# Kernel optimization log

Measured on AMD Instinct MI355X. Metric: run time of the kernel, lower is better.

The kernel has to match this reference:

```python
import jax, jax.numpy as jnp
import numpy as np
import math

D_MODEL = 1024
N_HEADS = 16
D_K = D_MODEL // N_HEADS
THRESH = 0.1  # attention probs below this are zeroed


def setup_inputs() -> dict:
    key = jax.random.key(0)
    ks = jax.random.split(key, 9)
    B, S, D = 2, 2048, D_MODEL
    scale = 1.0 / math.sqrt(D)
    x = jax.random.normal(ks[0], (B, S, D), dtype=jnp.float32)
    Wq = jax.random.normal(ks[1], (D, D), dtype=jnp.float32) * scale
    bq = jax.random.normal(ks[2], (D,), dtype=jnp.float32) * 0.01
    Wk = jax.random.normal(ks[3], (D, D), dtype=jnp.float32) * scale
    bk = jax.random.normal(ks[4], (D,), dtype=jnp.float32) * 0.01
    Wv = jax.random.normal(ks[5], (D, D), dtype=jnp.float32) * scale
    bv = jax.random.normal(ks[6], (D,), dtype=jnp.float32) * 0.01
    Wo = jax.random.normal(ks[7], (D, D), dtype=jnp.float32) * scale
    bo = jax.random.normal(ks[8], (D,), dtype=jnp.float32) * 0.01
    return {"x": x, "Wq": Wq, "bq": bq, "Wk": Wk, "bk": bk,
            "Wv": Wv, "bv": bv, "Wo": Wo, "bo": bo}


def _split_heads(t):
    B, S, D = t.shape
    return t.reshape(B, S, N_HEADS, D_K).transpose(0, 2, 1, 3)  # [B,H,S,dk]


def reference(x, Wq, bq, Wk, bk, Wv, bv, Wo, bo):
    # torch nn.Linear: y = x @ W.T + b
    q = _split_heads(x @ Wq.T + bq)
    k = _split_heads(x @ Wk.T + bk)
    v = _split_heads(x @ Wv.T + bv)
    scores = jnp.einsum('bhqd,bhkd->bhqk', q, k) / math.sqrt(D_K)
    probs = jax.nn.softmax(scores, axis=-1)          # full unmasked softmax (returned)
    keep = probs >= THRESH                            # ~low_attention_mask
    probs_model = jnp.where(keep, probs, 0.0)        # masked_fill; dropout is identity in eval
    ctx = jnp.einsum('bhqk,bhkd->bhqd', probs_model, v)
    B, H, S, dk = ctx.shape
    merged = ctx.transpose(0, 2, 1, 3).reshape(B, S, H * dk)
    out = merged @ Wo.T + bo
    attention_sum = probs.sum(axis=1)                # [B,S,S] sum over heads
    attention_mask = keep.astype(jnp.float32).sum(axis=1)  # [B,S,S]
    return (out, attention_sum, attention_mask)
```

## Files before the change

### kernel.cpp

```cpp
#include <hip/hip_runtime.h>

#define SDIM 2048
#define DDIM 1024
#define NH 16
#define DK 64
#define NB 2
#define MROWS (NB * SDIM)
#define MAXEV 65536
#define EXPC 0.18033688011112f

typedef _Float16 f16x8 __attribute__((ext_vector_type(8)));
typedef _Float16 f16x4 __attribute__((ext_vector_type(4)));
typedef float f32x4 __attribute__((ext_vector_type(4)));

__device__ __forceinline__ void ld_lds16(const _Float16* g, _Float16* l) {
  __builtin_amdgcn_global_load_lds(
      (const __attribute__((address_space(1))) void*)g,
      (__attribute__((address_space(3))) void*)l, 16, 0, 0);
}

__global__ __launch_bounds__(256) void cvt_f16(
    const float* __restrict__ x, const float* __restrict__ wq,
    const float* __restrict__ wk, const float* __restrict__ wv,
    _Float16* __restrict__ xh, _Float16* __restrict__ wqh,
    _Float16* __restrict__ wkh, _Float16* __restrict__ wvh) {
  int i = blockIdx.x * 256 + threadIdx.x;
  const float* src;
  _Float16* dst;
  int off;
  if (i < 1048576) {
    src = x; dst = xh; off = i;
  } else if (i < 1310720) {
    src = wq; dst = wqh; off = i - 1048576;
  } else if (i < 1572864) {
    src = wk; dst = wkh; off = i - 1310720;
  } else {
    src = wv; dst = wvh; off = i - 1572864;
  }
  float4 v = ((const float4*)src)[off];
  f16x4 h;
  h[0] = (_Float16)v.x; h[1] = (_Float16)v.y;
  h[2] = (_Float16)v.z; h[3] = (_Float16)v.w;
  ((f16x4*)dst)[off] = h;
}

__global__ __launch_bounds__(256, 2) void proj_gemm(
    const _Float16* __restrict__ xh, const _Float16* __restrict__ Wqh,
    const _Float16* __restrict__ Wkh, const _Float16* __restrict__ Wvh,
    const float* __restrict__ bq, const float* __restrict__ bk,
    const float* __restrict__ bv, _Float16* __restrict__ Qo,
    _Float16* __restrict__ Ko, float* __restrict__ Vo) {
  __shared__ _Float16 sA[128 * 64];
  __shared__ _Float16 sB[128 * 64];
  const int t = threadIdx.x;
  const int lane = t & 63, wv = t >> 6;
  const int lr = lane & 15, quad = lane >> 4;
  const int wm = wv >> 1, wn = wv & 1;
  const int m0 = blockIdx.y * 128, n0 = blockIdx.x * 128;
  const int z = blockIdx.z;
  const _Float16* Bp = z == 0 ? Wqh : (z == 1 ? Wkh : Wvh);
  const float* bias = z == 0 ? bq : (z == 1 ? bk : bv);

  const int strow = t >> 3;
  const int stchunk = t & 7;
  const int stsrc = (stchunk ^ (strow & 7)) * 8;

  f32x4 acc[4][4];
#pragma unroll
  for (int i = 0; i < 4; ++i)
#pragma unroll
    for (int j = 0; j < 4; ++j) acc[i][j] = (f32x4){0.f, 0.f, 0.f, 0.f};

  for (int k0 = 0; k0 < DDIM; k0 += 64) {
    __syncthreads();
#pragma unroll
    for (int i = 0; i < 4; ++i) {
      const int row = i * 32 + strow;
      ld_lds16(&xh[(size_t)(m0 + row) * DDIM + k0 + stsrc],
               &sA[row * 64 + stchunk * 8]);
      ld_lds16(&Bp[(size_t)(n0 + row) * DDIM + k0 + stsrc],
               &sB[row * 64 + stchunk * 8]);
    }
    __syncthreads();
    f16x8 af[4][2], bf[4][2];
#pragma unroll
    for (int i = 0; i < 4; ++i)
#pragma unroll
      for (int kk = 0; kk < 2; ++kk) {
        const int ph = ((kk * 4 + quad) ^ (lr & 7)) * 8;
        af[i][kk] = *(const f16x8*)&sA[(wm * 64 + i * 16 + lr) * 64 + ph];
        bf[i][kk] = *(const f16x8*)&sB[(wn * 64 + i * 16 + lr) * 64 + ph];
      }
#pragma unroll
    for (int kk = 0; kk < 2; ++kk)
#pragma unroll
      for (int i = 0; i < 4; ++i)
#pragma unroll
        for (int j = 0; j < 4; ++j)
          acc[i][j] = __builtin_amdgcn_mfma_f32_16x16x32_f16(
              af[i][kk], bf[j][kk], acc[i][j], 0, 0, 0);
  }
#pragma unroll
  for (int j = 0; j < 4; ++j) {
    const int ng = n0 + wn * 64 + j * 16 + lr;
    const float bvv = bias[ng];
    const int h = ng >> 6, d = ng & 63;
#pragma unroll
    for (int i = 0; i < 4; ++i) {
#pragma unroll
      for (int r = 0; r < 4; ++r) {
        const int mg = m0 + wm * 64 + i * 16 + quad * 4 + r;
        const int b = mg >> 11, s = mg & 2047;
        const float o = acc[i][j][r] + bvv;
        const size_t off = ((size_t)(b * NH + h) * SDIM + s) * DK + d;
        if (z == 0)
          Qo[off] = (_Float16)o;
        else if (z == 1)
          Ko[off] = (_Float16)o;
        else
          Vo[off] = o;
      }
    }
  }
}

__global__ __launch_bounds__(256) void attn_denom(const _Float16* __restrict__ Q,
                                                  const _Float16* __restrict__ K,
                                                  float* __restrict__ invDen) {
  __shared__ _Float16 Kbuf[2 * 64 * 64];
  const int t = threadIdx.x;
  const int lane = t & 63, wave = t >> 6;
  const int quad = lane >> 4, lr = lane & 15;
  const int q0 = blockIdx.x * 64;
  const int bh = blockIdx.y;
  const _Float16* Qh = Q + (size_t)bh * SDIM * DK;
  const _Float16* Kh = K + (size_t)bh * SDIM * DK;
  const size_t qoff = (size_t)(q0 + wave * 16 + lr) * DK + quad * 8;
  const f16x8 aq0 = *(const f16x8*)&Qh[qoff];
  const f16x8 aq1 = *(const f16x8*)&Qh[qoff + 32];
  const int strow = t >> 3, stchunk = t & 7;
  const int stsrc = (stchunk ^ (strow & 7)) * 8;
  const int ph0 = (quad ^ (lr & 7)) * 8;
  const int ph1 = ((4 + quad) ^ (lr & 7)) * 8;

  float dsum[4] = {0.f, 0.f, 0.f, 0.f};
#pragma unroll
  for (int i = 0; i < 2; ++i)
    ld_lds16(&Kh[(size_t)(i * 32 + strow) * DK + stsrc],
             &Kbuf[(i * 32 + strow) * 64 + stchunk * 8]);

  for (int kt = 0; kt < 32; ++kt) {
    __syncthreads();
    if (kt + 1 < 32) {
      const int kn = (kt + 1) * 64;
      const int bsel = ((kt + 1) & 1) * 4096;
#pragma unroll
      for (int i = 0; i < 2; ++i)
        ld_lds16(&Kh[(size_t)(kn + i * 32 + strow) * DK + stsrc],
                 &Kbuf[bsel + (i * 32 + strow) * 64 + stchunk * 8]);
    }
    const _Float16* Ks = &Kbuf[(kt & 1) * 4096];
#pragma unroll
    for (int c = 0; c < 4; ++c) {
      f16x8 b0 = *(const f16x8*)&Ks[(c * 16 + lr) * 64 + ph0];
      f16x8 b1 = *(const f16x8*)&Ks[(c * 16 + lr) * 64 + ph1];
      f32x4 acc = {0.f, 0.f, 0.f, 0.f};
      acc = __builtin_amdgcn_mfma_f32_16x16x32_f16(aq0, b0, acc, 0, 0, 0);
      acc = __builtin_amdgcn_mfma_f32_16x16x32_f16(aq1, b1, acc, 0, 0, 0);
#pragma unroll
      for (int r = 0; r < 4; ++r)
        dsum[r] += exp2f(acc[r] * EXPC);
    }
  }
#pragma unroll
  for (int m = 1; m < 16; m <<= 1)
#pragma unroll
    for (int r = 0; r < 4; ++r)
      dsum[r] += __shfl_xor(dsum[r], m, 64);
  if (lr == 0) {
#pragma unroll
    for (int r = 0; r < 4; ++r)
      invDen[(size_t)bh * SDIM + q0 + wave * 16 + quad * 4 + r] =
          1.0f / dsum[r];
  }
}

__global__ __launch_bounds__(256) void attn_pass2(
    const _Float16* __restrict__ Q, const _Float16* __restrict__ K,
    const float* __restrict__ invDen, float* __restrict__ attSum,
    float* __restrict__ attMask, float4* __restrict__ ev,
    int* __restrict__ ecnt) {
  __shared__ float Tbuf[64 * 68];
  _Float16* Kbuf = (_Float16*)Tbuf;
  const int t = threadIdx.x;
  const int lane = t & 63, wave = t >> 6;
  const int quad = lane >> 4, lr = lane & 15;
  const int k0 = blockIdx.x * 64;
  const int q0 = blockIdx.y * 64;
  const int b = blockIdx.z;
  const int strow = t >> 3, stchunk = t & 7;
  const int stsrc = (stchunk ^ (strow & 7)) * 8;
  const int ph0 = (quad ^ (lr & 7)) * 8;
  const int ph1 = ((4 + quad) ^ (lr & 7)) * 8;

  const size_t qbase = ((size_t)(b * NH) * SDIM + q0 + wave * 16 + lr) * DK;
  const size_t dbase = (size_t)(b * NH) * SDIM + q0 + wave * 16 + quad * 4;
  const size_t hstep = (size_t)SDIM * DK;

  float asum[4][4] = {};
  float amask[4][4] = {};

  {
    const _Float16* Kh = K + (size_t)(b * NH) * hstep + (size_t)k0 * DK;
#pragma unroll
    for (int i = 0; i < 2; ++i)
      ld_lds16(&Kh[(size_t)(i * 32 + strow) * DK + stsrc],
               &Kbuf[(i * 32 + strow) * 64 + stchunk * 8]);
  }
  f16x8 aq0n = *(const f16x8*)&Q[qbase + quad * 8];
  f16x8 aq1n = *(const f16x8*)&Q[qbase + 32 + quad * 8];
  float4 iln = *(const float4*)&invDen[dbase];

#pragma unroll 1
  for (int h = 0; h < NH; ++h) {
    const f16x8 aq0 = aq0n, aq1 = aq1n;
    const float4 il4 = iln;
    __syncthreads();
    if (h + 1 < NH) {
      const _Float16* Kn =
          K + (size_t)(b * NH + h + 1) * hstep + (size_t)k0 * DK;
      const int bsel = ((h + 1) & 1) * 4096;
#pragma unroll
      for (int i = 0; i < 2; ++i)
        ld_lds16(&Kn[(size_t)(i * 32 + strow) * DK + stsrc],
                 &Kbuf[bsel + (i * 32 + strow) * 64 + stchunk * 8]);
      aq0n = *(const f16x8*)&Q[qbase + (size_t)(h + 1) * hstep + quad * 8];
      aq1n = *(const f16x8*)&Q[qbase + (size_t)(h + 1) * hstep + 32 + quad * 8];
      iln = *(const float4*)&invDen[dbase + (size_t)(h + 1) * SDIM];
    }
    const _Float16* Ks = &Kbuf[(h & 1) * 4096];
    const float il[4] = {il4.x, il4.y, il4.z, il4.w};
#pragma unroll
    for (int c = 0; c < 4; ++c) {
      f16x8 b0 = *(const f16x8*)&Ks[(c * 16 + lr) * 64 + ph0];
      f16x8 b1 = *(const f16x8*)&Ks[(c * 16 + lr) * 64 + ph1];
      f32x4 acc = {0.f, 0.f, 0.f, 0.f};
      acc = __builtin_amdgcn_mfma_f32_16x16x32_f16(aq0, b0, acc, 0, 0, 0);
      acc = __builtin_amdgcn_mfma_f32_16x16x32_f16(aq1, b1, acc, 0, 0, 0);
#pragma unroll
      for (int r = 0; r < 4; ++r) {
        float p = exp2f(acc[r] * EXPC) * il[r];
        asum[c][r] += p;
        if (p >= 0.1f) {
          amask[c][r] += 1.0f;
          int idx = atomicAdd(ecnt, 1);
          if (idx < MAXEV)
            ev[idx] = make_float4(
                __int_as_float(b * NH + h),
                __int_as_float(q0 + wave * 16 + quad * 4 + r),
                __int_as_float(k0 + c * 16 + lr), p);
        }
      }
    }
  }
  const int orow = t >> 2, ocol = (t & 3) * 16;
  __syncthreads();
#pragma unroll
  for (int c = 0; c < 4; ++c)
#pragma unroll
    for (int r = 0; r < 4; ++r)
      Tbuf[(wave * 16 + quad * 4 + r) * 68 + c * 16 + lr] = asum[c][r];
  __syncthreads();
#pragma unroll
  for (int j = 0; j < 4; ++j) {
    float4 v = *(float4*)&Tbuf[orow * 68 + ocol + j * 4];
    *(float4*)&attSum[((size_t)(b * SDIM) + q0 + orow) * SDIM + k0 + ocol +
                      j * 4] = v;
  }
  __syncthreads();
#pragma unroll
  for (int c = 0; c < 4; ++c)
#pragma unroll
    for (int r = 0; r < 4; ++r)
      Tbuf[(wave * 16 + quad * 4 + r) * 68 + c * 16 + lr] = amask[c][r];
  __syncthreads();
#pragma unroll
  for (int j = 0; j < 4; ++j) {
    float4 v = *(float4*)&Tbuf[orow * 68 + ocol + j * 4];
    *(float4*)&attMask[((size_t)(b * SDIM) + q0 + orow) * SDIM + k0 + ocol +
                       j * 4] = v;
  }
}

__global__ __launch_bounds__(64) void apply_events(
    const float4* __restrict__ ev, const int* __restrict__ ecnt,
    const float* __restrict__ V, float* __restrict__ merged,
    int* __restrict__ flags) {
  int n = *ecnt;
  if (n > MAXEV) n = MAXEV;
  const int d = threadIdx.x;
  for (int e = blockIdx.x; e < n; e += gridDim.x) {
    float4 r = ev[e];
    int bh = __float_as_int(r.x);
    int q = __float_as_int(r.y);
    int kc = __float_as_int(r.z);
    float p = r.w;
    int b = bh >> 4, h = bh & 15;
    atomicAdd(&merged[((size_t)(b * SDIM + q)) * DDIM + h * DK + d],
              p * V[((size_t)bh * SDIM + kc) * DK + d]);
    if (d == 0) flags[b * SDIM + q] = 1;
  }
}

__global__ __launch_bounds__(256) void out_gemm(const float* __restrict__ A,
                                                const float* __restrict__ W,
                                                const float* __restrict__ bias,
                                                float* __restrict__ out,
                                                const int* __restrict__ flags) {
  __shared__ float As[16][68];
  __shared__ float Ws[16][68];
  __shared__ int anyF;
  const int t = threadIdx.x;
  const int tx = t & 15, ty = t >> 4;
  const int m0 = blockIdx.y * 64;
  const int n0 = blockIdx.x * 64;
  if (t == 0) anyF = 0;
  __syncthreads();
  if (t < 64 && flags[m0 + t]) anyF = 1;
  __syncthreads();
  const int nb = n0 + tx * 4;
  const float4 bv = *(const float4*)&bias[nb];
  if (!anyF) {
#pragma unroll
    for (int r = 0; r < 4; ++r)
      *(float4*)&out[(size_t)(m0 + ty * 4 + r) * DDIM + nb] = bv;
    return;
  }
  const int lr = t >> 2;
  const int lc = (t & 3) * 4;
  float acc[4][4] = {};
  for (int k0 = 0; k0 < DDIM; k0 += 16) {
    __syncthreads();
    float4 av = *(const float4*)&A[(size_t)(m0 + lr) * DDIM + k0 + lc];
    float4 wv = *(const float4*)&W[(size_t)(n0 + lr) * DDIM + k0 + lc];
    As[lc + 0][lr] = av.x; As[lc + 1][lr] = av.y;
    As[lc + 2][lr] = av.z; As[lc + 3][lr] = av.w;
    Ws[lc + 0][lr] = wv.x; Ws[lc + 1][lr] = wv.y;
    Ws[lc + 2][lr] = wv.z; Ws[lc + 3][lr] = wv.w;
    __syncthreads();
#pragma unroll
    for (int kk = 0; kk < 16; ++kk) {
      float4 a4 = *(const float4*)&As[kk][ty * 4];
      float4 b4 = *(const float4*)&Ws[kk][tx * 4];
      const float a[4] = {a4.x, a4.y, a4.z, a4.w};
      const float b[4] = {b4.x, b4.y, b4.z, b4.w};
#pragma unroll
      for (int r = 0; r < 4; ++r)
#pragma unroll
        for (int c = 0; c < 4; ++c)
          acc[r][c] = fmaf(a[r], b[c], acc[r][c]);
    }
  }
#pragma unroll
  for (int r = 0; r < 4; ++r) {
    float4 o;
    o.x = acc[r][0] + bv.x;
    o.y = acc[r][1] + bv.y;
    o.z = acc[r][2] + bv.z;
    o.w = acc[r][3] + bv.w;
    *(float4*)&out[(size_t)(m0 + ty * 4 + r) * DDIM + nb] = o;
  }
}

extern "C" void kernel_launch(void* const* d_in, const int* in_sizes, int n_in,
                              void* d_out, int out_size, void* d_ws,
                              size_t ws_size, hipStream_t stream) {
  const float* x = (const float*)d_in[0];
  const float* Wq = (const float*)d_in[1];
  const float* bq = (const float*)d_in[2];
  const float* Wk = (const float*)d_in[3];
  const float* bk = (const float*)d_in[4];
  const float* Wv = (const float*)d_in[5];
  const float* bv = (const float*)d_in[6];
  const float* Wo = (const float*)d_in[7];
  const float* bo = (const float*)d_in[8];

  float* out = (float*)d_out;
  float* attSum = out + (size_t)MROWS * DDIM;
  float* attMask = attSum + (size_t)NB * SDIM * SDIM;

  char* ws = (char*)d_ws;
  const size_t bigF = (size_t)MROWS * DDIM * sizeof(float);
  const size_t bigH = (size_t)MROWS * DDIM * sizeof(_Float16);
  const size_t wH = (size_t)DDIM * DDIM * sizeof(_Float16);
  _Float16* Qh = (_Float16*)ws;  ws += bigH;
  _Float16* Kh = (_Float16*)ws;  ws += bigH;
  float* V = (float*)ws;         ws += bigF;
  float* merged = (float*)ws;    ws += bigF;
  _Float16* xh = (_Float16*)ws;  ws += bigH;
  _Float16* Wqh = (_Float16*)ws; ws += wH;
  _Float16* Wkh = (_Float16*)ws; ws += wH;
  _Float16* Wvh = (_Float16*)ws; ws += wH;
  float* invDen = (float*)ws;    ws += (size_t)NB * NH * SDIM * sizeof(float);
  float4* ev = (float4*)ws;      ws += (size_t)MAXEV * sizeof(float4);
  int* flags = (int*)ws;         ws += (size_t)MROWS * sizeof(int);
  int* ecnt = (int*)ws;          ws += 16;

  hipMemsetAsync(merged, 0, bigF, stream);
  hipMemsetAsync(flags, 0, (size_t)MROWS * sizeof(int), stream);
  hipMemsetAsync(ecnt, 0, 16, stream);

  dim3 blk(256);
  cvt_f16<<<dim3(7168), blk, 0, stream>>>(x, Wq, Wk, Wv, xh, Wqh, Wkh, Wvh);
  proj_gemm<<<dim3(8, 32, 3), blk, 0, stream>>>(xh, Wqh, Wkh, Wvh, bq, bk, bv,
                                                Qh, Kh, V);
  attn_denom<<<dim3(32, 32), blk, 0, stream>>>(Qh, Kh, invDen);
  attn_pass2<<<dim3(32, 32, 2), blk, 0, stream>>>(Qh, Kh, invDen, attSum,
                                                  attMask, ev, ecnt);
  apply_events<<<dim3(256), dim3(64), 0, stream>>>(ev, ecnt, V, merged, flags);
  out_gemm<<<dim3(16, 64), blk, 0, stream>>>(merged, Wo, bo, out, flags);
}
```

Before: 289.0 us.

## Drop LDS staging of K in attention kernels and hoist rare-event path

Both attention kernels now read K fragments straight from global memory into MFMA operands instead of double-buffering them through LDS, which removes the barriers and LDS traffic. The threshold-event emission in pass2 moves out of the hot loop into a wave-uniform branch that recomputes the scores only when some lane has a hit. exp2f is swapped for the hardware exp2 builtin, and the denom grid is reordered so blocks sharing a head run close together. The trade-off is more redundant global/L2 reads of K per wave, plus recomputation on the rare hit path.

```diff
diff --git a/kernel.cpp b/kernel.cpp
--- a/kernel.cpp
+++ b/kernel.cpp
@@ -127,50 +127,27 @@
 __global__ __launch_bounds__(256) void attn_denom(const _Float16* __restrict__ Q,
                                                   const _Float16* __restrict__ K,
                                                   float* __restrict__ invDen) {
-  __shared__ _Float16 Kbuf[2 * 64 * 64];
   const int t = threadIdx.x;
   const int lane = t & 63, wave = t >> 6;
   const int quad = lane >> 4, lr = lane & 15;
-  const int q0 = blockIdx.x * 64;
-  const int bh = blockIdx.y;
+  const int bh = blockIdx.x;
+  const int q0 = blockIdx.y * 64;
   const _Float16* Qh = Q + (size_t)bh * SDIM * DK;
   const _Float16* Kh = K + (size_t)bh * SDIM * DK;
   const size_t qoff = (size_t)(q0 + wave * 16 + lr) * DK + quad * 8;
   const f16x8 aq0 = *(const f16x8*)&Qh[qoff];
   const f16x8 aq1 = *(const f16x8*)&Qh[qoff + 32];
-  const int strow = t >> 3, stchunk = t & 7;
-  const int stsrc = (stchunk ^ (strow & 7)) * 8;
-  const int ph0 = (quad ^ (lr & 7)) * 8;
-  const int ph1 = ((4 + quad) ^ (lr & 7)) * 8;
-
   float dsum[4] = {0.f, 0.f, 0.f, 0.f};
-#pragma unroll
-  for (int i = 0; i < 2; ++i)
-    ld_lds16(&Kh[(size_t)(i * 32 + strow) * DK + stsrc],
-             &Kbuf[(i * 32 + strow) * 64 + stchunk * 8]);
-
-  for (int kt = 0; kt < 32; ++kt) {
-    __syncthreads();
-    if (kt + 1 < 32) {
-      const int kn = (kt + 1) * 64;
-      const int bsel = ((kt + 1) & 1) * 4096;
-#pragma unroll
-      for (int i = 0; i < 2; ++i)
-        ld_lds16(&Kh[(size_t)(kn + i * 32 + strow) * DK + stsrc],
-                 &Kbuf[bsel + (i * 32 + strow) * 64 + stchunk * 8]);
-    }
-    const _Float16* Ks = &Kbuf[(kt & 1) * 4096];
-#pragma unroll
-    for (int c = 0; c < 4; ++c) {
-      f16x8 b0 = *(const f16x8*)&Ks[(c * 16 + lr) * 64 + ph0];
-      f16x8 b1 = *(const f16x8*)&Ks[(c * 16 + lr) * 64 + ph1];
-      f32x4 acc = {0.f, 0.f, 0.f, 0.f};
-      acc = __builtin_amdgcn_mfma_f32_16x16x32_f16(aq0, b0, acc, 0, 0, 0);
-      acc = __builtin_amdgcn_mfma_f32_16x16x32_f16(aq1, b1, acc, 0, 0, 0);
-#pragma unroll
-      for (int r = 0; r < 4; ++r)
-        dsum[r] += exp2f(acc[r] * EXPC);
-    }
+#pragma unroll 4
+  for (int k = 0; k < SDIM; k += 16) {
+    const f16x8 b0 = *(const f16x8*)&Kh[(size_t)(k + lr) * DK + quad * 8];
+    const f16x8 b1 = *(const f16x8*)&Kh[(size_t)(k + lr) * DK + 32 + quad * 8];
+    f32x4 acc = {0.f, 0.f, 0.f, 0.f};
+    acc = __builtin_amdgcn_mfma_f32_16x16x32_f16(aq0, b0, acc, 0, 0, 0);
+    acc = __builtin_amdgcn_mfma_f32_16x16x32_f16(aq1, b1, acc, 0, 0, 0);
+#pragma unroll
+    for (int r = 0; r < 4; ++r)
+      dsum[r] += __builtin_amdgcn_exp2f(acc[r] * EXPC);
   }
 #pragma unroll
   for (int m = 1; m < 16; m <<= 1)
@@ -191,17 +168,12 @@
     float* __restrict__ attMask, float4* __restrict__ ev,
     int* __restrict__ ecnt) {
   __shared__ float Tbuf[64 * 68];
-  _Float16* Kbuf = (_Float16*)Tbuf;
   const int t = threadIdx.x;
   const int lane = t & 63, wave = t >> 6;
   const int quad = lane >> 4, lr = lane & 15;
   const int k0 = blockIdx.x * 64;
   const int q0 = blockIdx.y * 64;
   const int b = blockIdx.z;
-  const int strow = t >> 3, stchunk = t & 7;
-  const int stsrc = (stchunk ^ (strow & 7)) * 8;
-  const int ph0 = (quad ^ (lr & 7)) * 8;
-  const int ph1 = ((4 + quad) ^ (lr & 7)) * 8;
 
   const size_t qbase = ((size_t)(b * NH) * SDIM + q0 + wave * 16 + lr) * DK;
   const size_t dbase = (size_t)(b * NH) * SDIM + q0 + wave * 16 + quad * 4;
@@ -210,13 +182,6 @@
   float asum[4][4] = {};
   float amask[4][4] = {};
 
-  {
-    const _Float16* Kh = K + (size_t)(b * NH) * hstep + (size_t)k0 * DK;
-#pragma unroll
-    for (int i = 0; i < 2; ++i)
-      ld_lds16(&Kh[(size_t)(i * 32 + strow) * DK + stsrc],
-               &Kbuf[(i * 32 + strow) * 64 + stchunk * 8]);
-  }
   f16x8 aq0n = *(const f16x8*)&Q[qbase + quad * 8];
   f16x8 aq1n = *(const f16x8*)&Q[qbase + 32 + quad * 8];
   float4 iln = *(const float4*)&invDen[dbase];
@@ -225,40 +190,49 @@
   for (int h = 0; h < NH; ++h) {
     const f16x8 aq0 = aq0n, aq1 = aq1n;
     const float4 il4 = iln;
-    __syncthreads();
     if (h + 1 < NH) {
-      const _Float16* Kn =
-          K + (size_t)(b * NH + h + 1) * hstep + (size_t)k0 * DK;
-      const int bsel = ((h + 1) & 1) * 4096;
-#pragma unroll
-      for (int i = 0; i < 2; ++i)
-        ld_lds16(&Kn[(size_t)(i * 32 + strow) * DK + stsrc],
-                 &Kbuf[bsel + (i * 32 + strow) * 64 + stchunk * 8]);
       aq0n = *(const f16x8*)&Q[qbase + (size_t)(h + 1) * hstep + quad * 8];
       aq1n = *(const f16x8*)&Q[qbase + (size_t)(h + 1) * hstep + 32 + quad * 8];
       iln = *(const float4*)&invDen[dbase + (size_t)(h + 1) * SDIM];
     }
-    const _Float16* Ks = &Kbuf[(h & 1) * 4096];
+    const _Float16* Kp = K + (size_t)(b * NH + h) * hstep + (size_t)k0 * DK;
     const float il[4] = {il4.x, il4.y, il4.z, il4.w};
+    int anyh = 0;
 #pragma unroll
     for (int c = 0; c < 4; ++c) {
-      f16x8 b0 = *(const f16x8*)&Ks[(c * 16 + lr) * 64 + ph0];
-      f16x8 b1 = *(const f16x8*)&Ks[(c * 16 + lr) * 64 + ph1];
+      const f16x8 b0 = *(const f16x8*)&Kp[(c * 16 + lr) * DK + quad * 8];
+      const f16x8 b1 = *(const f16x8*)&Kp[(c * 16 + lr) * DK + 32 + quad * 8];
       f32x4 acc = {0.f, 0.f, 0.f, 0.f};
       acc = __builtin_amdgcn_mfma_f32_16x16x32_f16(aq0, b0, acc, 0, 0, 0);
       acc = __builtin_amdgcn_mfma_f32_16x16x32_f16(aq1, b1, acc, 0, 0, 0);
 #pragma unroll
       for (int r = 0; r < 4; ++r) {
-        float p = exp2f(acc[r] * EXPC) * il[r];
+        const float p = __builtin_amdgcn_exp2f(acc[r] * EXPC) * il[r];
         asum[c][r] += p;
-        if (p >= 0.1f) {
-          amask[c][r] += 1.0f;
-          int idx = atomicAdd(ecnt, 1);
-          if (idx < MAXEV)
-            ev[idx] = make_float4(
-                __int_as_float(b * NH + h),
-                __int_as_float(q0 + wave * 16 + quad * 4 + r),
-                __int_as_float(k0 + c * 16 + lr), p);
+        const int hit = p >= 0.1f;
+        amask[c][r] += (float)hit;
+        anyh |= hit;
+      }
+    }
+    if (__any(anyh)) {
+#pragma unroll 1
+      for (int c = 0; c < 4; ++c) {
+        const f16x8 b0 = *(const f16x8*)&Kp[(c * 16 + lr) * DK + quad * 8];
+        const f16x8 b1 = *(const f16x8*)&Kp[(c * 16 + lr) * DK + 32 + quad * 8];
+        f32x4 acc = {0.f, 0.f, 0.f, 0.f};
+        acc = __builtin_amdgcn_mfma_f32_16x16x32_f16(aq0, b0, acc, 0, 0, 0);
+        acc = __builtin_amdgcn_mfma_f32_16x16x32_f16(aq1, b1, acc, 0, 0, 0);
+#pragma unroll 1
+        for (int r = 0; r < 4; ++r) {
+          const float p = __builtin_amdgcn_exp2f(acc[r] * EXPC) * il[r];
+          if (p >= 0.1f) {
+            int idx = atomicAdd(ecnt, 1);
+            if (idx < MAXEV)
+              ev[idx] = make_float4(
+                  __int_as_float(b * NH + h),
+                  __int_as_float(q0 + wave * 16 + quad * 4 + r),
+                  __int_as_float(k0 + c * 16 + lr), p);
+          }
         }
       }
     }
```

After: 435.0 us. 50.6% more time.

## Fold softmax scale into Q, use log-denominator, split rare threshold pass

Applied to the files above, without the earlier changes.

The softmax scale and log2(e) factor are folded into Q at projection time. The denominator is now stored as a negative log2, so probabilities become a single exp2 of (score + bias) with no multiply. attn_pass2 loads K for two heads per sync, tracks the per-lane max exponent argument, and runs the mask/event-recording loop only when some lane could reach the 0.1 threshold. This takes the atomics and branching out of the hot loop, but the rare pass recomputes its MFMAs from global memory. attn_denom switches to single-buffered 128-row K tiles, which drops its load/compute overlap, and rounding Q to f16 after scaling changes precision slightly.

```diff
diff --git a/kernel.cpp b/kernel.cpp
--- a/kernel.cpp
+++ b/kernel.cpp
@@ -8,6 +8,7 @@
 #define MROWS (NB * SDIM)
 #define MAXEV 65536
 #define EXPC 0.18033688011112f
+#define L01 -3.3219281f
 
 typedef _Float16 f16x8 __attribute__((ext_vector_type(8)));
 typedef _Float16 f16x4 __attribute__((ext_vector_type(4)));
@@ -114,7 +115,7 @@
         const float o = acc[i][j][r] + bvv;
         const size_t off = ((size_t)(b * NH + h) * SDIM + s) * DK + d;
         if (z == 0)
-          Qo[off] = (_Float16)o;
+          Qo[off] = (_Float16)(o * EXPC);
         else if (z == 1)
           Ko[off] = (_Float16)o;
         else
@@ -126,8 +127,8 @@
 
 __global__ __launch_bounds__(256) void attn_denom(const _Float16* __restrict__ Q,
                                                   const _Float16* __restrict__ K,
-                                                  float* __restrict__ invDen) {
-  __shared__ _Float16 Kbuf[2 * 64 * 64];
+                                                  float* __restrict__ laOut) {
+  __shared__ _Float16 Ks[128 * 64];
   const int t = threadIdx.x;
   const int lane = t & 63, wave = t >> 6;
   const int quad = lane >> 4, lr = lane & 15;
@@ -144,24 +145,16 @@
   const int ph1 = ((4 + quad) ^ (lr & 7)) * 8;
 
   float dsum[4] = {0.f, 0.f, 0.f, 0.f};
-#pragma unroll
-  for (int i = 0; i < 2; ++i)
-    ld_lds16(&Kh[(size_t)(i * 32 + strow) * DK + stsrc],
-             &Kbuf[(i * 32 + strow) * 64 + stchunk * 8]);
-
-  for (int kt = 0; kt < 32; ++kt) {
-    __syncthreads();
-    if (kt + 1 < 32) {
-      const int kn = (kt + 1) * 64;
-      const int bsel = ((kt + 1) & 1) * 4096;
-#pragma unroll
-      for (int i = 0; i < 2; ++i)
-        ld_lds16(&Kh[(size_t)(kn + i * 32 + strow) * DK + stsrc],
-                 &Kbuf[bsel + (i * 32 + strow) * 64 + stchunk * 8]);
-    }
-    const _Float16* Ks = &Kbuf[(kt & 1) * 4096];
-#pragma unroll
-    for (int c = 0; c < 4; ++c) {
+#pragma unroll 1
+  for (int kt = 0; kt < 16; ++kt) {
+    __syncthreads();
+#pragma unroll
+    for (int i = 0; i < 4; ++i)
+      ld_lds16(&Kh[(size_t)(kt * 128 + i * 32 + strow) * DK + stsrc],
+               &Ks[(i * 32 + strow) * 64 + stchunk * 8]);
+    __syncthreads();
+#pragma unroll
+    for (int c = 0; c < 8; ++c) {
       f16x8 b0 = *(const f16x8*)&Ks[(c * 16 + lr) * 64 + ph0];
       f16x8 b1 = *(const f16x8*)&Ks[(c * 16 + lr) * 64 + ph1];
       f32x4 acc = {0.f, 0.f, 0.f, 0.f};
@@ -169,7 +162,7 @@
       acc = __builtin_amdgcn_mfma_f32_16x16x32_f16(aq1, b1, acc, 0, 0, 0);
 #pragma unroll
       for (int r = 0; r < 4; ++r)
-        dsum[r] += exp2f(acc[r] * EXPC);
+        dsum[r] += __builtin_amdgcn_exp2f(acc[r]);
     }
   }
 #pragma unroll
@@ -180,18 +173,19 @@
   if (lr == 0) {
 #pragma unroll
     for (int r = 0; r < 4; ++r)
-      invDen[(size_t)bh * SDIM + q0 + wave * 16 + quad * 4 + r] =
-          1.0f / dsum[r];
+      laOut[(size_t)bh * SDIM + q0 + wave * 16 + quad * 4 + r] =
+          -__builtin_amdgcn_logf(dsum[r]);
   }
 }
 
 __global__ __launch_bounds__(256) void attn_pass2(
     const _Float16* __restrict__ Q, const _Float16* __restrict__ K,
-    const float* __restrict__ invDen, float* __restrict__ attSum,
+    const float* __restrict__ la, float* __restrict__ attSum,
     float* __restrict__ attMask, float4* __restrict__ ev,
     int* __restrict__ ecnt) {
-  __shared__ float Tbuf[64 * 68];
-  _Float16* Kbuf = (_Float16*)Tbuf;
+  __shared__ float SMEM[64 * 68];
+  _Float16* Khs = (_Float16*)SMEM;
+  float* Tbuf = SMEM;
   const int t = threadIdx.x;
   const int lane = t & 63, wave = t >> 6;
   const int quad = lane >> 4, lr = lane & 15;
@@ -209,56 +203,79 @@
 
   float asum[4][4] = {};
   float amask[4][4] = {};
-
-  {
-    const _Float16* Kh = K + (size_t)(b * NH) * hstep + (size_t)k0 * DK;
-#pragma unroll
-    for (int i = 0; i < 2; ++i)
-      ld_lds16(&Kh[(size_t)(i * 32 + strow) * DK + stsrc],
-               &Kbuf[(i * 32 + strow) * 64 + stchunk * 8]);
-  }
-  f16x8 aq0n = *(const f16x8*)&Q[qbase + quad * 8];
-  f16x8 aq1n = *(const f16x8*)&Q[qbase + 32 + quad * 8];
-  float4 iln = *(const float4*)&invDen[dbase];
+  float mx = -1e30f;
 
 #pragma unroll 1
-  for (int h = 0; h < NH; ++h) {
-    const f16x8 aq0 = aq0n, aq1 = aq1n;
-    const float4 il4 = iln;
-    __syncthreads();
-    if (h + 1 < NH) {
-      const _Float16* Kn =
-          K + (size_t)(b * NH + h + 1) * hstep + (size_t)k0 * DK;
-      const int bsel = ((h + 1) & 1) * 4096;
+  for (int hp = 0; hp < 8; ++hp) {
+    __syncthreads();
+#pragma unroll
+    for (int hh = 0; hh < 2; ++hh) {
+      const _Float16* Kp =
+          K + (size_t)(b * NH + 2 * hp + hh) * hstep + (size_t)k0 * DK;
 #pragma unroll
       for (int i = 0; i < 2; ++i)
-        ld_lds16(&Kn[(size_t)(i * 32 + strow) * DK + stsrc],
-                 &Kbuf[bsel + (i * 32 + strow) * 64 + stchunk * 8]);
-      aq0n = *(const f16x8*)&Q[qbase + (size_t)(h + 1) * hstep + quad * 8];
-      aq1n = *(const f16x8*)&Q[qbase + (size_t)(h + 1) * hstep + 32 + quad * 8];
-      iln = *(const float4*)&invDen[dbase + (size_t)(h + 1) * SDIM];
-    }
-    const _Float16* Ks = &Kbuf[(h & 1) * 4096];
-    const float il[4] = {il4.x, il4.y, il4.z, il4.w};
-#pragma unroll
-    for (int c = 0; c < 4; ++c) {
-      f16x8 b0 = *(const f16x8*)&Ks[(c * 16 + lr) * 64 + ph0];
-      f16x8 b1 = *(const f16x8*)&Ks[(c * 16 + lr) * 64 + ph1];
-      f32x4 acc = {0.f, 0.f, 0.f, 0.f};
-      acc = __builtin_amdgcn_mfma_f32_16x16x32_f16(aq0, b0, acc, 0, 0, 0);
-      acc = __builtin_amdgcn_mfma_f32_16x16x32_f16(aq1, b1, acc, 0, 0, 0);
-#pragma unroll
-      for (int r = 0; r < 4; ++r) {
-        float p = exp2f(acc[r] * EXPC) * il[r];
-        asum[c][r] += p;
-        if (p >= 0.1f) {
-          amask[c][r] += 1.0f;
-          int idx = atomicAdd(ecnt, 1);
-          if (idx < MAXEV)
-            ev[idx] = make_float4(
-                __int_as_float(b * NH + h),
-                __int_as_float(q0 + wave * 16 + quad * 4 + r),
-                __int_as_float(k0 + c * 16 + lr), p);
+        ld_lds16(&Kp[(size_t)(i * 32 + strow) * DK + stsrc],
+                 &Khs[hh * 4096 + (i * 32 + strow) * 64 + stchunk * 8]);
+    }
+    f16x8 a0[2], a1[2];
+    float4 lav[2];
+#pragma unroll
+    for (int hh = 0; hh < 2; ++hh) {
+      const size_t ho = (size_t)(2 * hp + hh) * hstep;
+      a0[hh] = *(const f16x8*)&Q[qbase + ho + quad * 8];
+      a1[hh] = *(const f16x8*)&Q[qbase + ho + 32 + quad * 8];
+      lav[hh] = *(const float4*)&la[dbase + (size_t)(2 * hp + hh) * SDIM];
+    }
+    __syncthreads();
+#pragma unroll
+    for (int hh = 0; hh < 2; ++hh) {
+      const _Float16* Ks = &Khs[hh * 4096];
+      const float lar[4] = {lav[hh].x, lav[hh].y, lav[hh].z, lav[hh].w};
+#pragma unroll
+      for (int c = 0; c < 4; ++c) {
+        f16x8 b0 = *(const f16x8*)&Ks[(c * 16 + lr) * 64 + ph0];
+        f16x8 b1 = *(const f16x8*)&Ks[(c * 16 + lr) * 64 + ph1];
+        f32x4 acc = {0.f, 0.f, 0.f, 0.f};
+        acc = __builtin_amdgcn_mfma_f32_16x16x32_f16(a0[hh], b0, acc, 0, 0, 0);
+        acc = __builtin_amdgcn_mfma_f32_16x16x32_f16(a1[hh], b1, acc, 0, 0, 0);
+#pragma unroll
+        for (int r = 0; r < 4; ++r) {
+          const float arg = acc[r] + lar[r];
+          mx = fmaxf(mx, arg);
+          asum[c][r] += __builtin_amdgcn_exp2f(arg);
+        }
+      }
+    }
+  }
+  if (__any(mx >= L01)) {
+#pragma unroll 1
+    for (int h = 0; h < NH; ++h) {
+      const _Float16* Kp =
+          K + (size_t)(b * NH + h) * hstep + (size_t)k0 * DK;
+      const size_t ho = (size_t)h * hstep;
+      const f16x8 aq0 = *(const f16x8*)&Q[qbase + ho + quad * 8];
+      const f16x8 aq1 = *(const f16x8*)&Q[qbase + ho + 32 + quad * 8];
+      const float4 l4 = *(const float4*)&la[dbase + (size_t)h * SDIM];
+      const float lar[4] = {l4.x, l4.y, l4.z, l4.w};
+#pragma unroll 1
+      for (int c = 0; c < 4; ++c) {
+        const f16x8 b0 = *(const f16x8*)&Kp[(c * 16 + lr) * DK + quad * 8];
+        const f16x8 b1 = *(const f16x8*)&Kp[(c * 16 + lr) * DK + 32 + quad * 8];
+        f32x4 acc = {0.f, 0.f, 0.f, 0.f};
+        acc = __builtin_amdgcn_mfma_f32_16x16x32_f16(aq0, b0, acc, 0, 0, 0);
+        acc = __builtin_amdgcn_mfma_f32_16x16x32_f16(aq1, b1, acc, 0, 0, 0);
+#pragma unroll 1
+        for (int r = 0; r < 4; ++r) {
+          const float p = __builtin_amdgcn_exp2f(acc[r] + lar[r]);
+          if (p >= 0.1f) {
+            amask[c][r] += 1.0f;
+            int idx = atomicAdd(ecnt, 1);
+            if (idx < MAXEV)
+              ev[idx] = make_float4(
+                  __int_as_float(b * NH + h),
+                  __int_as_float(q0 + wave * 16 + quad * 4 + r),
+                  __int_as_float(k0 + c * 16 + lr), p);
+          }
         }
       }
     }
@@ -401,7 +418,7 @@
   _Float16* Wqh = (_Float16*)ws; ws += wH;
   _Float16* Wkh = (_Float16*)ws; ws += wH;
   _Float16* Wvh = (_Float16*)ws; ws += wH;
-  float* invDen = (float*)ws;    ws += (size_t)NB * NH * SDIM * sizeof(float);
+  float* laBuf = (float*)ws;     ws += (size_t)NB * NH * SDIM * sizeof(float);
   float4* ev = (float4*)ws;      ws += (size_t)MAXEV * sizeof(float4);
   int* flags = (int*)ws;         ws += (size_t)MROWS * sizeof(int);
   int* ecnt = (int*)ws;          ws += 16;
@@ -414,8 +431,8 @@
   cvt_f16<<<dim3(7168), blk, 0, stream>>>(x, Wq, Wk, Wv, xh, Wqh, Wkh, Wvh);
   proj_gemm<<<dim3(8, 32, 3), blk, 0, stream>>>(xh, Wqh, Wkh, Wvh, bq, bk, bv,
                                                 Qh, Kh, V);
-  attn_denom<<<dim3(32, 32), blk, 0, stream>>>(Qh, Kh, invDen);
-  attn_pass2<<<dim3(32, 32, 2), blk, 0, stream>>>(Qh, Kh, invDen, attSum,
+  attn_denom<<<dim3(32, 32), blk, 0, stream>>>(Qh, Kh, laBuf);
+  attn_pass2<<<dim3(32, 32, 2), blk, 0, stream>>>(Qh, Kh, laBuf, attSum,
                                                   attMask, ev, ecnt);
   apply_events<<<dim3(256), dim3(64), 0, stream>>>(ev, ecnt, V, merged, flags);
   out_gemm<<<dim3(16, 64), blk, 0, stream>>>(merged, Wo, bo, out, flags);
```

New measurement: 250.7 us. 13.2% less time.
